# Kernel optimization log

Hardware: AMD Instinct MI355X
Metric: run time of the kernel (lower is better)

The kernel has to match this reference:

```python
import jax, jax.numpy as jnp
import numpy as np

SHARPNESS = 1000.0   # sigmoid temperature from source: *1000.0
BIAS = 0.008         # shadow acne bias from source: -0.008
FILTER_SIZE = 1      # 3x3 PCF
SHADOW_STEP = 1


def setup_inputs() -> dict:
    key = jax.random.key(0)
    k1, k2, k3 = jax.random.split(key, 3)
    N, H, W, K, S = 8, 1024, 1024, 1, 2048
    # light-view depth buffer (fragments_from_light.zbuf), K=1 squeezed
    light_zbuf = jax.random.uniform(k1, (N, S, S), dtype=jnp.float32)
    depth_z = jax.random.uniform(k2, (N, H, W, K), dtype=jnp.float32)
    # rounded integer light-screen coords per camera pixel: [..., 0]=x, [..., 1]=y
    xy = jax.random.randint(k3, (N, H, W, K, 2), 0, S, dtype=jnp.int32)
    return {"light_zbuf": light_zbuf, "depth_z": depth_z, "xy": xy, "image_size": S}


def reference(light_zbuf, depth_z, xy, image_size):
    N, H, W, K = depth_z.shape
    b = jnp.arange(N, dtype=jnp.int32)[:, None, None, None]  # broadcast batch index
    x = xy[..., 0]  # [N,H,W,K]
    y = xy[..., 1]
    aa = depth_z - BIAS
    vis = jnp.zeros_like(depth_z)
    # 3x3 PCF: gather clamped neighbors in the light zbuf, soft depth test, accumulate
    for ii in range(-FILTER_SIZE, FILTER_SIZE + 1):
        for jj in range(-FILTER_SIZE, FILTER_SIZE + 1):
            yi = jnp.clip(y + ii * SHADOW_STEP, 0, image_size - 1)
            xi = jnp.clip(x + jj * SHADOW_STEP, 0, image_size - 1)
            bb = light_zbuf[b, yi, xi]  # [N,H,W,K] gather
            vis = vis + jax.nn.sigmoid((bb - aa) * SHARPNESS)
    return vis / float((1 + 2 * FILTER_SIZE) ** 2)
```

## Files before the change

### kernel.cpp

```cpp
#include <hip/hip_runtime.h>


#define SHARPNESS 1000.0f
#define BIAS 0.008f
#define S2LOG2E 1442.6950408889634f

#define S_IMG   2048
#define NBATCH  8
#define HWK     (1 << 20)
#define TSH     6
#define TPS     32
#define BPB     (TPS * TPS)
#define CAP     1280
#define STW     66
#define PXB     16384
#define SENT    0xFFFFFFFFu

typedef int      i4v __attribute__((ext_vector_type(4)));
typedef float    f2v __attribute__((ext_vector_type(2)));
typedef float    f4v __attribute__((ext_vector_type(4)));
typedef unsigned u2v __attribute__((ext_vector_type(2)));

__device__ __forceinline__ float sigf(float bb, float a) {
    const float t = (a - bb) * S2LOG2E;
    return __builtin_amdgcn_rcpf(1.0f + exp2f(t));
}

__global__ __launch_bounds__(1024, 2) void p1_bin(
    const int* __restrict__ xy_raw, const float* __restrict__ depth,
    u2v* __restrict__ slab, unsigned* __restrict__ pidx,
    unsigned* __restrict__ gcur, int b0)
{
    __shared__ unsigned cnt[BPB];
    __shared__ unsigned cur[BPB];
    const int blk = blockIdx.x;
    const int bl  = blk >> 6;
    const int sub = blk & 63;
    const int tid = threadIdx.x;
    cnt[tid] = 0;
    __syncthreads();

    const size_t pb_g = ((size_t)(b0 + bl)) * HWK + (size_t)sub * PXB;
    const i4v* xq = (const i4v*)xy_raw + pb_g / 2;
    const f2v* dq = (const f2v*)depth  + pb_g / 2;

    unsigned pk[16]; float dd[16];
#pragma unroll
    for (int j = 0; j < 8; ++j) {
        const i4v q = __builtin_nontemporal_load(&xq[j * 1024 + tid]);
        const f2v d = __builtin_nontemporal_load(&dq[j * 1024 + tid]);
        pk[2 * j]     = (unsigned)q.x | ((unsigned)q.y << 11);
        pk[2 * j + 1] = (unsigned)q.z | ((unsigned)q.w << 11);
        dd[2 * j] = d.x; dd[2 * j + 1] = d.y;
        atomicAdd(&cnt[((q.y >> TSH) << 5) | (q.x >> TSH)], 1u);
        atomicAdd(&cnt[((q.w >> TSH) << 5) | (q.z >> TSH)], 1u);
    }
    __syncthreads();
    cur[tid] = atomicAdd(&gcur[bl * BPB + tid], cnt[tid]);
    __syncthreads();

    const size_t pb_l = (size_t)bl * HWK + (size_t)sub * PXB;
    u2v* px2 = (u2v*)pidx + pb_l / 2;
#pragma unroll
    for (int j = 0; j < 8; ++j) {
        u2v pi;
#pragma unroll
        for (int e = 0; e < 2; ++e) {
            const unsigned w = pk[2 * j + e];
            const int x = (int)(w & 0x7FFu), y = (int)(w >> 11);
            const int bn = ((y >> TSH) << 5) | (x >> TSH);
            const unsigned pos = atomicAdd(&cur[bn], 1u);
            unsigned v = SENT;
            if (pos < CAP) {
                const unsigned slot = (unsigned)(bl * BPB + bn) * CAP + pos;
                u2v r;
                r.x = (unsigned)(x & 63) | ((unsigned)(y & 63) << 6);
                r.y = __float_as_uint(dd[2 * j + e]);
                slab[slot] = r;
                v = slot;
            }
            if (e == 0) pi.x = v; else pi.y = v;
        }
        px2[j * 1024 + tid] = pi;
    }
}

__global__ __launch_bounds__(256, 8) void p2_tile(
    const float* __restrict__ zbuf, u2v* __restrict__ slab,
    const unsigned* __restrict__ gcur, int b0)
{
    __shared__ float zt[STW * STW];
    const int gb  = blockIdx.x;
    const int tid = threadIdx.x;
    const int bl  = gb >> 10;
    const int t   = gb & (BPB - 1);
    const int tx  = t & 31, ty = t >> 5;
    const float* zb = zbuf + (size_t)(b0 + bl) * ((size_t)S_IMG * S_IMG);
    const int x0 = tx * 64 - 1, y0 = ty * 64 - 1;

    const int n   = min((int)gcur[gb], CAP);
    const int nc  = n - 1;
    const int ncc = max(nc, 0);
    u2v* sl = slab + (size_t)gb * CAP;

    u2v Rc[5];
#pragma unroll
    for (int j = 0; j < 5; ++j)
        Rc[j] = sl[min(j * 256 + tid, ncc)];

    for (int i = tid; i < STW * STW; i += 256) {
        const int r  = i / STW, c = i - r * STW;
        const int gy = min(max(y0 + r, 0), S_IMG - 1);
        const int gx = min(max(x0 + c, 0), S_IMG - 1);
        zt[i] = zb[(size_t)gy * S_IMG + gx];
    }
    __syncthreads();

    float* slf = (float*)sl;
#pragma unroll
    for (int j = 0; j < 5; ++j) {
        const unsigned w = Rc[j].x;
        const float a  = __uint_as_float(Rc[j].y) - BIAS;
        const float* p = zt + (int)((w >> 6) & 63u) * STW + (int)(w & 63u);
        const float vis =
              sigf(p[0],           a) + sigf(p[1],           a) + sigf(p[2],           a)
            + sigf(p[STW],         a) + sigf(p[STW + 1],     a) + sigf(p[STW + 2],     a)
            + sigf(p[2 * STW],     a) + sigf(p[2 * STW + 1], a) + sigf(p[2 * STW + 2], a);
        const int k = j * 256 + tid;
        if (k <= nc) slf[2 * k + 1] = vis * (1.0f / 9.0f);
    }
}

__global__ __launch_bounds__(256) void p3_out(
    const unsigned* __restrict__ pidx, const float* __restrict__ slabf,
    float* __restrict__ out,
    const float* __restrict__ zbuf, const float* __restrict__ depth,
    const int* __restrict__ xy_raw, int b0)
{
    const int tid = threadIdx.x;
    const i4v* px4 = (const i4v*)pidx;
    const size_t gbase = (size_t)blockIdx.x * 1024;

    i4v P[4];
#pragma unroll
    for (int j = 0; j < 4; ++j)
        P[j] = __builtin_nontemporal_load(&px4[gbase + j * 256 + tid]);

    f4v V[4];
#pragma unroll
    for (int j = 0; j < 4; ++j) {
#pragma unroll
        for (int e = 0; e < 4; ++e) {
            const unsigned pi = (unsigned)P[j][e];
            float v;
            if (pi != SENT) {
                v = slabf[2 * (size_t)pi + 1];
            } else {
                const size_t il = (size_t)b0 * HWK + (gbase + j * 256 + tid) * 4 + e;
                const int batch = (int)(il >> 20);
                const float a = depth[il] - BIAS;
                const int x = xy_raw[2 * il], y = xy_raw[2 * il + 1];
                const float* zbb = zbuf + (size_t)batch * ((size_t)S_IMG * S_IMG);
                float vv = 0.0f;
                for (int ii = -1; ii <= 1; ++ii) {
                    const int yi = min(max(y + ii, 0), S_IMG - 1);
                    const float* row = zbb + (size_t)yi * S_IMG;
                    for (int jj = -1; jj <= 1; ++jj)
                        vv += sigf(row[min(max(x + jj, 0), S_IMG - 1)], a);
                }
                v = vv * (1.0f / 9.0f);
            }
            V[j][e] = v;
        }
    }

    f4v* o4 = (f4v*)(out + (size_t)b0 * HWK);
#pragma unroll
    for (int j = 0; j < 4; ++j)
        __builtin_nontemporal_store(V[j], &o4[gbase + j * 256 + tid]);
}

__global__ __launch_bounds__(256) void pcf_shadow_generic(
    const float* __restrict__ zbuf, const float* __restrict__ depth_z,
    const int2* __restrict__ xy, const int* __restrict__ image_size_p,
    float* __restrict__ out, int total, int zbuf_elems)
{
    const int i = blockIdx.x * blockDim.x + threadIdx.x;
    if (i >= total) return;
    const int S  = *image_size_p;
    const int SS = S * S;
    const int N  = zbuf_elems / SS;
    const int hwk = total / N;
    const int b   = i / hwk;
    const float a = depth_z[i] - BIAS;
    const int2 p  = xy[i];
    const float* base = zbuf + (size_t)b * (size_t)SS;
    float vis = 0.0f;
#pragma unroll
    for (int ii = -1; ii <= 1; ++ii) {
        const int yi = min(max(p.y + ii, 0), S - 1);
        const float* row = base + (size_t)yi * (size_t)S;
#pragma unroll
        for (int jj = -1; jj <= 1; ++jj) {
            const int xi = min(max(p.x + jj, 0), S - 1);
            vis += 1.0f / (1.0f + __expf((a - row[xi]) * SHARPNESS));
        }
    }
    out[i] = vis * (1.0f / 9.0f);
}

extern "C" void kernel_launch(void* const* d_in, const int* in_sizes, int n_in,
                              void* d_out, int out_size, void* d_ws, size_t ws_size,
                              hipStream_t stream) {
    const float* zbuf     = (const float*)d_in[0];
    const float* depth_z  = (const float*)d_in[1];
    const int*   xy_raw   = (const int*)d_in[2];
    const int*   img_size = (const int*)d_in[3];
    float*       out      = (float*)d_out;

    const int zbuf_elems = in_sizes[0];
    const int total      = in_sizes[1];

    if (zbuf_elems == NBATCH * S_IMG * S_IMG && total == NBATCH * HWK) {
        const size_t per_b = (size_t)BPB * CAP * 8ull + (size_t)HWK * 4ull
                           + (size_t)BPB * 4ull;
        int nb = 0;
        if      (ws_size >= 8 * per_b) nb = 8;
        else if (ws_size >= 4 * per_b) nb = 4;
        else if (ws_size >= 2 * per_b) nb = 2;
        else if (ws_size >= 1 * per_b) nb = 1;

        if (nb) {
            const size_t slab_b = (size_t)nb * BPB * CAP * 8ull;
            const size_t pidx_b = (size_t)nb * HWK * 4ull;
            u2v*      slab = (u2v*)d_ws;
            unsigned* pidx = (unsigned*)((char*)d_ws + slab_b);
            unsigned* gcur = (unsigned*)((char*)d_ws + slab_b + pidx_b);
            for (int b0 = 0; b0 < NBATCH; b0 += nb) {
                hipMemsetAsync(gcur, 0, (size_t)nb * BPB * 4ull, stream);
                p1_bin<<<nb * 64,  1024, 0, stream>>>(xy_raw, depth_z, slab, pidx, gcur, b0);
                p2_tile<<<nb * BPB, 256, 0, stream>>>(zbuf, slab, gcur, b0);
                p3_out<<<nb * 256,  256, 0, stream>>>(pidx, (const float*)slab, out,
                                                      zbuf, depth_z, xy_raw, b0);
            }
            return;
        }
    }
    const int block = 256;
    const int grid  = (total + block - 1) / block;
    pcf_shadow_generic<<<grid, block, 0, stream>>>(zbuf, depth_z, (const int2*)xy_raw,
                                                   img_size, out, total, zbuf_elems);
}
```

Measured before the change: 432.8 us.

## Stage binned records in LDS, write coalesced slab runs, store indices in output

The binning kernel now does a local prefix scan over tile counts and first places each record in shared memory. Each wave then copies per-tile runs to the global slab contiguously, padded to multiples of eight, instead of scattering one record per atomic. The per-pixel slot index is written into the output buffer itself rather than a separate pidx array. Visibility values go to a separate compact array, and CAP and records-per-thread are raised to match. This trades extra LDS traffic, scan barriers and padding for coalesced global writes and less workspace traffic.

Result: faster. 394.4 us (-8.9%).

```diff
diff --git a/kernel.cpp b/kernel.cpp
--- a/kernel.cpp
+++ b/kernel.cpp
@@ -11,83 +11,118 @@
 #define TSH     6
 #define TPS     32
 #define BPB     (TPS * TPS)
-#define CAP     1280
+#define CAP     1792
+#define RPT     7
 #define STW     66
-#define PXB     16384
+#define PXB     8192
+#define P1T     1024
+#define PPT     (PXB / P1T)
 #define SENT    0xFFFFFFFFu
 
 typedef int      i4v __attribute__((ext_vector_type(4)));
 typedef float    f2v __attribute__((ext_vector_type(2)));
 typedef float    f4v __attribute__((ext_vector_type(4)));
 typedef unsigned u2v __attribute__((ext_vector_type(2)));
+typedef unsigned u4v __attribute__((ext_vector_type(4)));
 
 __device__ __forceinline__ float sigf(float bb, float a) {
     const float t = (a - bb) * S2LOG2E;
     return __builtin_amdgcn_rcpf(1.0f + exp2f(t));
 }
 
-__global__ __launch_bounds__(1024, 2) void p1_bin(
+__global__ __launch_bounds__(P1T, 2) void p1_bin(
     const int* __restrict__ xy_raw, const float* __restrict__ depth,
-    u2v* __restrict__ slab, unsigned* __restrict__ pidx,
+    u2v* __restrict__ slab, float* __restrict__ out ,
     unsigned* __restrict__ gcur, int b0)
 {
-    __shared__ unsigned cnt[BPB];
-    __shared__ unsigned cur[BPB];
+    __shared__ u2v      srec[PXB];
+    __shared__ unsigned scn[BPB];
+    __shared__ unsigned lbase[BPB];
+    __shared__ unsigned gbse[BPB];
+
     const int blk = blockIdx.x;
-    const int bl  = blk >> 6;
-    const int sub = blk & 63;
+    const int bl  = blk >> 7;
+    const int sub = blk & 127;
     const int tid = threadIdx.x;
-    cnt[tid] = 0;
-    __syncthreads();
-
-    const size_t pb_g = ((size_t)(b0 + bl)) * HWK + (size_t)sub * PXB;
+    scn[tid] = 0;
+    __syncthreads();
+
+    const size_t pb_g = (size_t)(b0 + bl) * HWK + (size_t)sub * PXB;
     const i4v* xq = (const i4v*)xy_raw + pb_g / 2;
     const f2v* dq = (const f2v*)depth  + pb_g / 2;
 
-    unsigned pk[16]; float dd[16];
-#pragma unroll
-    for (int j = 0; j < 8; ++j) {
-        const i4v q = __builtin_nontemporal_load(&xq[j * 1024 + tid]);
-        const f2v d = __builtin_nontemporal_load(&dq[j * 1024 + tid]);
+    unsigned pk[PPT]; float dd[PPT];
+#pragma unroll
+    for (int j = 0; j < PPT / 2; ++j) {
+        const i4v q = __builtin_nontemporal_load(&xq[j * P1T + tid]);
+        const f2v d = __builtin_nontemporal_load(&dq[j * P1T + tid]);
         pk[2 * j]     = (unsigned)q.x | ((unsigned)q.y << 11);
         pk[2 * j + 1] = (unsigned)q.z | ((unsigned)q.w << 11);
         dd[2 * j] = d.x; dd[2 * j + 1] = d.y;
-        atomicAdd(&cnt[((q.y >> TSH) << 5) | (q.x >> TSH)], 1u);
-        atomicAdd(&cnt[((q.w >> TSH) << 5) | (q.z >> TSH)], 1u);
-    }
-    __syncthreads();
-    cur[tid] = atomicAdd(&gcur[bl * BPB + tid], cnt[tid]);
-    __syncthreads();
-
-    const size_t pb_l = (size_t)bl * HWK + (size_t)sub * PXB;
-    u2v* px2 = (u2v*)pidx + pb_l / 2;
-#pragma unroll
-    for (int j = 0; j < 8; ++j) {
+        atomicAdd(&scn[((q.y >> TSH) << 5) | (q.x >> TSH)], 1u);
+        atomicAdd(&scn[((q.w >> TSH) << 5) | (q.z >> TSH)], 1u);
+    }
+    __syncthreads();
+
+    const unsigned creg = scn[tid];
+    for (int ofs = 1; ofs < BPB; ofs <<= 1) {
+        const unsigned u = (tid >= ofs) ? scn[tid - ofs] : 0u;
+        __syncthreads();
+        scn[tid] += u;
+        __syncthreads();
+    }
+    const unsigned lb = scn[tid] - creg;
+    lbase[tid] = lb;
+    gbse[tid]  = atomicAdd(&gcur[bl * BPB + tid], (creg + 7u) & ~7u);
+    scn[tid]   = lb;
+    __syncthreads();
+
+    u2v* px2 = (u2v*)(out + pb_g);
+#pragma unroll
+    for (int j = 0; j < PPT / 2; ++j) {
         u2v pi;
 #pragma unroll
         for (int e = 0; e < 2; ++e) {
             const unsigned w = pk[2 * j + e];
             const int x = (int)(w & 0x7FFu), y = (int)(w >> 11);
             const int bn = ((y >> TSH) << 5) | (x >> TSH);
-            const unsigned pos = atomicAdd(&cur[bn], 1u);
-            unsigned v = SENT;
+            const unsigned r = atomicAdd(&scn[bn], 1u);
+            u2v rec;
+            rec.x = (unsigned)(x & 63) | ((unsigned)(y & 63) << 6);
+            rec.y = __float_as_uint(dd[2 * j + e]);
+            srec[r] = rec;
+            const unsigned pos = gbse[bn] + (r - lbase[bn]);
+            const unsigned slot = (pos < CAP)
+                ? (unsigned)(bl * BPB + bn) * CAP + pos : SENT;
+            if (e == 0) pi.x = slot; else pi.y = slot;
+        }
+        px2[j * P1T + tid] = pi;
+    }
+    __syncthreads();
+
+    const int wid = tid >> 6, lane = tid & 63;
+    u2v* slb = slab + (size_t)bl * BPB * CAP;
+    for (int bn = wid * 64; bn < wid * 64 + 64; ++bn) {
+        const int c   = (int)(scn[bn] - lbase[bn]);
+        const int len = (c + 7) & ~7;
+        const int src = (int)lbase[bn];
+        const int gp  = (int)gbse[bn];
+        u2v* dst = slb + (size_t)bn * CAP;
+        for (int k = lane; k < len; k += 64) {
+            const int pos = gp + k;
             if (pos < CAP) {
-                const unsigned slot = (unsigned)(bl * BPB + bn) * CAP + pos;
                 u2v r;
-                r.x = (unsigned)(x & 63) | ((unsigned)(y & 63) << 6);
-                r.y = __float_as_uint(dd[2 * j + e]);
-                slab[slot] = r;
-                v = slot;
+                if (k < c) r = srec[src + k];
+                else { r.x = 0u; r.y = 0x7F800000u; }
+                dst[pos] = r;
             }
-            if (e == 0) pi.x = v; else pi.y = v;
-        }
-        px2[j * 1024 + tid] = pi;
+        }
     }
 }
 
 __global__ __launch_bounds__(256, 8) void p2_tile(
-    const float* __restrict__ zbuf, u2v* __restrict__ slab,
-    const unsigned* __restrict__ gcur, int b0)
+    const float* __restrict__ zbuf, const u2v* __restrict__ slab,
+    float* __restrict__ vis, const unsigned* __restrict__ gcur, int b0)
 {
     __shared__ float zt[STW * STW];
     const int gb  = blockIdx.x;
@@ -101,11 +136,11 @@
     const int n   = min((int)gcur[gb], CAP);
     const int nc  = n - 1;
     const int ncc = max(nc, 0);
-    u2v* sl = slab + (size_t)gb * CAP;
-
-    u2v Rc[5];
-#pragma unroll
-    for (int j = 0; j < 5; ++j)
+    const u2v* sl = slab + (size_t)gb * CAP;
+
+    u2v Rc[RPT];
+#pragma unroll
+    for (int j = 0; j < RPT; ++j)
         Rc[j] = sl[min(j * 256 + tid, ncc)];
 
     for (int i = tid; i < STW * STW; i += 256) {
@@ -116,47 +151,46 @@
     }
     __syncthreads();
 
-    float* slf = (float*)sl;
-#pragma unroll
-    for (int j = 0; j < 5; ++j) {
+    float* vb = vis + (size_t)gb * CAP;
+#pragma unroll
+    for (int j = 0; j < RPT; ++j) {
         const unsigned w = Rc[j].x;
         const float a  = __uint_as_float(Rc[j].y) - BIAS;
         const float* p = zt + (int)((w >> 6) & 63u) * STW + (int)(w & 63u);
-        const float vis =
+        const float v =
               sigf(p[0],           a) + sigf(p[1],           a) + sigf(p[2],           a)
             + sigf(p[STW],         a) + sigf(p[STW + 1],     a) + sigf(p[STW + 2],     a)
             + sigf(p[2 * STW],     a) + sigf(p[2 * STW + 1], a) + sigf(p[2 * STW + 2], a);
         const int k = j * 256 + tid;
-        if (k <= nc) slf[2 * k + 1] = vis * (1.0f / 9.0f);
+        if (k <= nc) vb[k] = v * (1.0f / 9.0f);
     }
 }
 
 __global__ __launch_bounds__(256) void p3_out(
-    const unsigned* __restrict__ pidx, const float* __restrict__ slabf,
-    float* __restrict__ out,
+    const float* __restrict__ visf, float* __restrict__ out,
     const float* __restrict__ zbuf, const float* __restrict__ depth,
     const int* __restrict__ xy_raw, int b0)
 {
     const int tid = threadIdx.x;
-    const i4v* px4 = (const i4v*)pidx;
-    const size_t gbase = (size_t)blockIdx.x * 1024;
-
-    i4v P[4];
+    const size_t pxbase = (size_t)b0 * HWK + (size_t)blockIdx.x * 4096;
+    const u4v* px4 = (const u4v*)(out + pxbase);
+
+    u4v P[4];
 #pragma unroll
     for (int j = 0; j < 4; ++j)
-        P[j] = __builtin_nontemporal_load(&px4[gbase + j * 256 + tid]);
+        P[j] = px4[j * 256 + tid];
 
     f4v V[4];
 #pragma unroll
     for (int j = 0; j < 4; ++j) {
 #pragma unroll
         for (int e = 0; e < 4; ++e) {
-            const unsigned pi = (unsigned)P[j][e];
+            const unsigned pi = P[j][e];
             float v;
             if (pi != SENT) {
-                v = slabf[2 * (size_t)pi + 1];
+                v = visf[pi];
             } else {
-                const size_t il = (size_t)b0 * HWK + (gbase + j * 256 + tid) * 4 + e;
+                const size_t il = pxbase + (size_t)(j * 256 + tid) * 4 + e;
                 const int batch = (int)(il >> 20);
                 const float a = depth[il] - BIAS;
                 const int x = xy_raw[2 * il], y = xy_raw[2 * il + 1];
@@ -174,10 +208,10 @@
         }
     }
 
-    f4v* o4 = (f4v*)(out + (size_t)b0 * HWK);
+    f4v* o4 = (f4v*)(out + pxbase);
 #pragma unroll
     for (int j = 0; j < 4; ++j)
-        __builtin_nontemporal_store(V[j], &o4[gbase + j * 256 + tid]);
+        __builtin_nontemporal_store(V[j], &o4[j * 256 + tid]);
 }
 
 __global__ __launch_bounds__(256) void pcf_shadow_generic(
@@ -222,8 +256,9 @@
     const int total      = in_sizes[1];
 
     if (zbuf_elems == NBATCH * S_IMG * S_IMG && total == NBATCH * HWK) {
-        const size_t per_b = (size_t)BPB * CAP * 8ull + (size_t)HWK * 4ull
-                           + (size_t)BPB * 4ull;
+        const size_t slab_pb = (size_t)BPB * CAP * 8ull;
+        const size_t vis_pb  = (size_t)BPB * CAP * 4ull;
+        const size_t per_b   = slab_pb + vis_pb + (size_t)BPB * 4ull;
         int nb = 0;
         if      (ws_size >= 8 * per_b) nb = 8;
         else if (ws_size >= 4 * per_b) nb = 4;
@@ -231,17 +266,14 @@
         else if (ws_size >= 1 * per_b) nb = 1;
 
         if (nb) {
-            const size_t slab_b = (size_t)nb * BPB * CAP * 8ull;
-            const size_t pidx_b = (size_t)nb * HWK * 4ull;
             u2v*      slab = (u2v*)d_ws;
-            unsigned* pidx = (unsigned*)((char*)d_ws + slab_b);
-            unsigned* gcur = (unsigned*)((char*)d_ws + slab_b + pidx_b);
+            float*    vis  = (float*)((char*)d_ws + (size_t)nb * slab_pb);
+            unsigned* gcur = (unsigned*)((char*)d_ws + (size_t)nb * (slab_pb + vis_pb));
             for (int b0 = 0; b0 < NBATCH; b0 += nb) {
                 hipMemsetAsync(gcur, 0, (size_t)nb * BPB * 4ull, stream);
-                p1_bin<<<nb * 64,  1024, 0, stream>>>(xy_raw, depth_z, slab, pidx, gcur, b0);
-                p2_tile<<<nb * BPB, 256, 0, stream>>>(zbuf, slab, gcur, b0);
-                p3_out<<<nb * 256,  256, 0, stream>>>(pidx, (const float*)slab, out,
-                                                      zbuf, depth_z, xy_raw, b0);
+                p1_bin <<<nb * 128, P1T, 0, stream>>>(xy_raw, depth_z, slab, out, gcur, b0);
+                p2_tile<<<nb * BPB, 256, 0, stream>>>(zbuf, slab, vis, gcur, b0);
+                p3_out <<<nb * 256, 256, 0, stream>>>(vis, out, zbuf, depth_z, xy_raw, b0);
             }
             return;
         }
```
